# Performance work log

Measured on AMD Instinct MI355X. Metric: run time of the kernel, lower is better.

## Reference

```python
import math
import jax, jax.numpy as jnp
import numpy as np

B, T, C, H = 2, 1024, 1024, 16
D = C // H          # head_dim = 64
ROPE_M = 32         # min(head_dim//2, 64)
FB_M = 32
ROPE_BASE = 10000.0


def setup_inputs() -> dict:
    key = jax.random.key(0)
    ks = jax.random.split(key, 8)
    x = jax.random.normal(ks[0], (B, T, C), dtype=jnp.float32)
    # default coords: per-token position, d_coord=1
    coords = jnp.broadcast_to(jnp.arange(T, dtype=jnp.float32)[None, :, None], (B, T, 1))
    # c_attn / c_proj linear params (torch Linear: y = x @ W.T + b)
    W_attn = jax.random.normal(ks[1], (3 * C, C), dtype=jnp.float32) * (1.0 / math.sqrt(C))
    b_attn = jnp.zeros((3 * C,), dtype=jnp.float32)
    W_proj = jax.random.normal(ks[2], (C, C), dtype=jnp.float32) * (1.0 / math.sqrt(C))
    b_proj = jnp.zeros((C,), dtype=jnp.float32)
    # RoPE freq bank, kind='log': exp(linspace(log(1/base), 0, m)) replicated over d_coord
    steps = jnp.exp(jnp.linspace(math.log(1.0 / ROPE_BASE), 0.0, ROPE_M)).astype(jnp.float32)
    W_rope = steps[:, None]  # [m, d_coord=1]
    # Fourier-bias bank, kind='gaussian', sigma=1.0
    W_fb = jax.random.normal(ks[3], (FB_M, 1), dtype=jnp.float32)
    # betas are zero-init nn.Parameters; use small random values so bias path is exercised
    beta_cos = jax.random.normal(ks[4], (FB_M,), dtype=jnp.float32) * 0.1
    beta_sin = jax.random.normal(ks[5], (FB_M,), dtype=jnp.float32) * 0.1
    return {"x": x, "coords": coords, "W_attn": W_attn, "b_attn": b_attn,
            "W_proj": W_proj, "b_proj": b_proj, "W_rope": W_rope, "W_fb": W_fb,
            "beta_cos": beta_cos, "beta_sin": beta_sin}


def _rope_rotate(z, c, s):
    # z: [B,H,T,D]; c,s: [B,1,T,ROPE_M]; rotates first 2*ROPE_M channels pairwise
    zr = z[..., :2 * ROPE_M].reshape(*z.shape[:-1], ROPE_M, 2)
    y0 = zr[..., 0] * c - zr[..., 1] * s
    y1 = zr[..., 0] * s + zr[..., 1] * c
    y = jnp.stack((y0, y1), axis=-1).reshape(*z.shape[:-1], 2 * ROPE_M)
    return jnp.concatenate([y, z[..., 2 * ROPE_M:]], axis=-1)


def reference(x, coords, W_attn, b_attn, W_proj, b_proj, W_rope, W_fb, beta_cos, beta_sin):
    qkv = x @ W_attn.T + b_attn                      # [B,T,3C]
    q, k, v = jnp.split(qkv, 3, axis=-1)
    to_heads = lambda z: z.reshape(B, T, H, D).transpose(0, 2, 1, 3)  # [B,H,T,D]
    q, k, v = to_heads(q), to_heads(k), to_heads(v)
    # Iron RoPE: theta = coords @ W_rope.T -> [B,T,ROPE_M]
    theta = coords @ W_rope.T
    c = jnp.cos(theta)[:, None]                      # [B,1,T,ROPE_M]
    s = jnp.sin(theta)[:, None]
    q = _rope_rotate(q, c, s)
    k = _rope_rotate(k, c, s)
    att = jnp.einsum('bhqd,bhkd->bhqk', q, k) * (1.0 / math.sqrt(D))
    # relative Fourier bias (shared across heads)
    delta = coords[:, :, None, :] - coords[:, None, :, :]   # [B,Tq,Tk,1]
    S = jnp.einsum('bqkd,md->bqkm', delta, W_fb)            # [B,Tq,Tk,FB_M]
    bias = (jnp.cos(S) * beta_cos + jnp.sin(S) * beta_sin).sum(-1)  # [B,Tq,Tk]
    att = att + (1.0 / math.sqrt(FB_M)) * bias[:, None]     # [B,H,Tq,Tk]
    # non-causal: mask buffer is all ones -> no masking; dropout p=0 -> identity
    att = jax.nn.softmax(att, axis=-1)
    y = jnp.einsum('bhqk,bhkd->bhqd', att, v)
    y = y.transpose(0, 2, 1, 3).reshape(B, T, C)
    y = y @ W_proj.T + b_proj
    return x + y
```

## Files before the change

### kernel.cpp

```cpp
#include <hip/hip_runtime.h>
#include <math.h>

#define Bc 2
#define Tc 1024
#define Cc 1024
#define Hc 16
#define Dc 64
#define DE 128

typedef unsigned short u16;
typedef __attribute__((ext_vector_type(8))) short bf16x8;
typedef __attribute__((ext_vector_type(4))) float f32x4;
typedef __attribute__((ext_vector_type(16))) float f32x16;

#define QSCALE 0.1803368801111243f
#define FIXED_M 24.0f

static __device__ inline u16 f2b(float f) {
    unsigned u = __float_as_uint(f);
    u = (u + 0x7fffu + ((u >> 16) & 1u)) >> 16;
    return (u16)u;
}
static __device__ inline float b2f(u16 h) {
    return __uint_as_float((unsigned)h << 16);
}

typedef __attribute__((address_space(1))) const unsigned int g_u32;
typedef __attribute__((address_space(3))) unsigned int l_u32;
static __device__ __forceinline__ void gll16(const void* g, void* l) {
    __builtin_amdgcn_global_load_lds((g_u32*)g, (l_u32*)l, 16, 0, 0);
}

__global__ __launch_bounds__(256) void cast_all(
    const float* __restrict__ x, const float* __restrict__ wa, const float* __restrict__ wp,
    u16* __restrict__ xb, u16* __restrict__ wab, u16* __restrict__ wpb)
{
    const int NX = Bc * Tc * Cc;
    const int NA = 3 * Cc * Cc;
    int i = (blockIdx.x * 256 + threadIdx.x) * 4;
    const float* src; u16* dst; int off;
    if (i < NX)            { src = x;  dst = xb;  off = i; }
    else if (i < NX + NA)  { src = wa; dst = wab; off = i - NX; }
    else                   { src = wp; dst = wpb; off = i - NX - NA; }
    float4 v = *(const float4*)(src + off);
    ushort4 o;
    o.x = f2b(v.x); o.y = f2b(v.y); o.z = f2b(v.z); o.w = f2b(v.w);
    *(ushort4*)(dst + off) = o;
}

template<int TM, int TN, int WR, int WC, bool OUT_BF16>
__global__ __launch_bounds__(256) void gemm_abt(
    const u16* __restrict__ A, const u16* __restrict__ Bm,
    const float* __restrict__ bias, const float* __restrict__ resid,
    float* __restrict__ outf, u16* __restrict__ outb, int M, int N, int K)
{
    constexpr int WTM = TM / WR;
    constexpr int WTN = TN / WC;
    constexpr int FI = WTM / 16;
    constexpr int FJ = WTN / 16;
    constexpr int ITA = TM / 32;
    constexpr int ITB = TN / 32;
    __shared__ u16 ldsA[2][TM * 64];
    __shared__ u16 ldsB[2][TN * 64];
    const int tid  = threadIdx.x;
    const int wave = tid >> 6;
    const int lane = tid & 63;
    const int l15  = lane & 15;
    const int quad = lane >> 4;
    const int wm = wave / WC;
    const int wn = wave % WC;
    const int tm = blockIdx.y * TM;
    const int tn = blockIdx.x * TN;

    f32x4 acc[FI][FJ] = {};

    auto stage = [&](int buf, int k0) {
#pragma unroll
        for (int it = 0; it < ITA; ++it) {
            int p = it * 256 + tid;
            int row = p >> 3;
            int c = ((p & 7) ^ (row & 7)) * 8;
            gll16(A + (size_t)(tm + row) * K + k0 + c,
                  &ldsA[buf][(it * 256 + (wave << 6)) * 8]);
        }
#pragma unroll
        for (int it = 0; it < ITB; ++it) {
            int p = it * 256 + tid;
            int row = p >> 3;
            int c = ((p & 7) ^ (row & 7)) * 8;
            gll16(Bm + (size_t)(tn + row) * K + k0 + c,
                  &ldsB[buf][(it * 256 + (wave << 6)) * 8]);
        }
    };

    const int NK = K >> 6;
    stage(0, 0);
    for (int ki = 0; ki < NK; ++ki) {
        const int buf = ki & 1;
        __syncthreads();
        if (ki + 1 < NK) stage(buf ^ 1, (ki + 1) << 6);
#pragma unroll
        for (int kk = 0; kk < 2; ++kk) {
            bf16x8 af[FI], bf[FJ];
#pragma unroll
            for (int i = 0; i < FI; ++i) {
                int row = wm * WTM + i * 16 + l15;
                int slot = (kk * 4 + quad) ^ (row & 7);
                af[i] = *(const bf16x8*)&ldsA[buf][row * 64 + slot * 8];
            }
#pragma unroll
            for (int j = 0; j < FJ; ++j) {
                int row = wn * WTN + j * 16 + l15;
                int slot = (kk * 4 + quad) ^ (row & 7);
                bf[j] = *(const bf16x8*)&ldsB[buf][row * 64 + slot * 8];
            }
#pragma unroll
            for (int i = 0; i < FI; ++i)
#pragma unroll
                for (int j = 0; j < FJ; ++j)
                    acc[i][j] = __builtin_amdgcn_mfma_f32_16x16x32_bf16(af[i], bf[j], acc[i][j], 0, 0, 0);
        }
    }

#pragma unroll
    for (int i = 0; i < FI; ++i) {
        int row = tm + wm * WTM + i * 16 + quad * 4;
#pragma unroll
        for (int j = 0; j < FJ; ++j) {
            int col = tn + wn * WTN + j * 16 + l15;
            float bb = bias[col];
#pragma unroll
            for (int r = 0; r < 4; ++r) {
                float v = acc[i][j][r] + bb;
                if (resid) v += resid[(size_t)(row + r) * N + col];
                if (OUT_BF16) outb[(size_t)(row + r) * N + col] = f2b(v);
                else          outf[(size_t)(row + r) * N + col] = v;
            }
        }
    }
}

__global__ __launch_bounds__(256) void prep_kernel(
    const u16* __restrict__ qkv, const float* __restrict__ coords,
    const float* __restrict__ W_rope, const float* __restrict__ W_fb,
    const float* __restrict__ bcos, const float* __restrict__ bsin,
    u16* __restrict__ qe, u16* __restrict__ ke, u16* __restrict__ vt)
{
    const int bt = blockIdx.x;
    const int b = bt >> 10;
    const int t = bt & (Tc - 1);
    const float coord = coords[bt];
    const int tid = threadIdx.x;
    const u16* row = qkv + (size_t)bt * 3072;
    const int e  = tid * 4;
    const int h  = e >> 6;
    const int d0 = e & 63;
    const int m0 = d0 >> 1;

    float th0 = coord * W_rope[m0];
    float th1 = coord * W_rope[m0 + 1];
    float s0 = sinf(th0), c0 = cosf(th0);
    float s1 = sinf(th1), c1 = cosf(th1);

    float q0 = b2f(row[e]), q1 = b2f(row[e + 1]), q2 = b2f(row[e + 2]), q3 = b2f(row[e + 3]);
    float k0 = b2f(row[1024 + e]), k1 = b2f(row[1025 + e]), k2 = b2f(row[1026 + e]), k3 = b2f(row[1027 + e]);
    float v0 = b2f(row[2048 + e]), v1 = b2f(row[2049 + e]), v2 = b2f(row[2050 + e]), v3 = b2f(row[2051 + e]);

    size_t qb = ((size_t)(b * Hc + h) * Tc + t) * DE + d0;
    qe[qb + 0] = f2b((q0 * c0 - q1 * s0) * QSCALE);
    qe[qb + 1] = f2b((q0 * s0 + q1 * c0) * QSCALE);
    qe[qb + 2] = f2b((q2 * c1 - q3 * s1) * QSCALE);
    qe[qb + 3] = f2b((q2 * s1 + q3 * c1) * QSCALE);
    ke[qb + 0] = f2b(k0 * c0 - k1 * s0);
    ke[qb + 1] = f2b(k0 * s0 + k1 * c0);
    ke[qb + 2] = f2b(k2 * c1 - k3 * s1);
    ke[qb + 3] = f2b(k2 * s1 + k3 * c1);

    size_t vb = ((size_t)(b * Hc + h) * Dc + d0) * Tc + t;
    vt[vb]          = f2b(v0);
    vt[vb + Tc]     = f2b(v1);
    vt[vb + 2 * Tc] = f2b(v2);
    vt[vb + 3 * Tc] = f2b(v3);

    {
        const int hh = tid >> 4;
        const int s  = tid & 15;
        const int m  = 2 * s;
        float thf0 = coord * W_fb[m],     thf1 = coord * W_fb[m + 1];
        float sn0 = sinf(thf0), cn0 = cosf(thf0);
        float sn1 = sinf(thf1), cn1 = cosf(thf1);
        float bc0 = bcos[m], bs0 = bsin[m], bc1 = bcos[m + 1], bs1 = bsin[m + 1];
        const float SC = 1.41421356237f * QSCALE;
        unsigned u1 = (unsigned)f2b((bc0 * cn0 + bs0 * sn0) * SC) |
                      ((unsigned)f2b((bc1 * cn1 + bs1 * sn1) * SC) << 16);
        unsigned u2 = (unsigned)f2b((bc0 * sn0 - bs0 * cn0) * SC) |
                      ((unsigned)f2b((bc1 * sn1 - bs1 * cn1) * SC) << 16);
        unsigned cp = (unsigned)f2b(cn0) | ((unsigned)f2b(cn1) << 16);
        unsigned sp = (unsigned)f2b(sn0) | ((unsigned)f2b(sn1) << 16);
        size_t base = ((size_t)(b * Hc + hh) * Tc + t) * DE + 64;
        *(unsigned*)&qe[base + m]      = u1;
        *(unsigned*)&qe[base + 32 + m] = u2;
        *(unsigned*)&ke[base + m]      = cp;
        *(unsigned*)&ke[base + 32 + m] = sp;
    }
}

__global__ __launch_bounds__(256) void attn_kernel(
    const u16* __restrict__ qe, const u16* __restrict__ ke,
    const u16* __restrict__ vt, u16* __restrict__ yb)
{
    __shared__ u16 ldsK[2][64 * 128];
    __shared__ u16 ldsV[2][64 * 64];
    __shared__ u16 plds[4][32][40];
    __shared__ float lM[2][32];
    const int tid  = threadIdx.x;
    const int wave = tid >> 6;
    const int lane = tid & 63;
    const int l31  = lane & 31;
    const int half = lane >> 5;
    const int qw = wave & 1;
    const int kw = wave >> 1;
    const int h  = blockIdx.x & 15;
    const int b  = blockIdx.x >> 4;
    const int qt = blockIdx.y * 64;

    const u16* Q  = qe + ((size_t)(b * Hc + h) * Tc) * DE;
    const u16* Kp = ke + ((size_t)(b * Hc + h) * Tc) * DE;
    const u16* Vp = vt + ((size_t)(b * Hc + h) * Dc) * Tc;

    bf16x8 qf[8];
    {
        const u16* qrow = Q + (size_t)(qt + qw * 32 + l31) * DE + half * 8;
#pragma unroll
        for (int c = 0; c < 8; ++c) qf[c] = *(const bf16x8*)(qrow + c * 16);
    }

    auto stageKV = [&](int buf, int kt) {
#pragma unroll
        for (int it = 0; it < 4; ++it) {
            int p = it * 256 + tid;
            int row = p >> 4;
            int c = (p & 15) ^ (row & 15);
            gll16(Kp + (size_t)(kt + row) * DE + c * 8,
                  &ldsK[buf][(it * 256 + (wave << 6)) * 8]);
        }
#pragma unroll
        for (int it = 0; it < 2; ++it) {
            int p = it * 256 + tid;
            int row = p >> 3;
            int c = (p & 7) ^ (row & 7);
            gll16(Vp + (size_t)row * Tc + kt + c * 8,
                  &ldsV[buf][(it * 256 + (wave << 6)) * 8]);
        }
    };

    f32x16 o[2] = {};
    float lrow[16] = {};

    stageKV(0, 0);
    for (int ki = 0; ki < Tc / 64; ++ki) {
        const int buf = ki & 1;
        __syncthreads();
        if (ki + 1 < Tc / 64) stageKV(buf ^ 1, (ki + 1) * 64);

        f32x16 sf = {};
#pragma unroll
        for (int c = 0; c < 8; ++c) {
            int row = kw * 32 + l31;
            int slot = (c * 2 + half) ^ (row & 15);
            bf16x8 kf = *(const bf16x8*)&ldsK[buf][row * 128 + slot * 8];
            sf = __builtin_amdgcn_mfma_f32_32x32x16_bf16(qf[c], kf, sf, 0, 0, 0);
        }
#pragma unroll
        for (int r = 0; r < 16; ++r) {
            float p = __builtin_amdgcn_exp2f(sf[r] - FIXED_M);
            u16 tp = (u16)(__float_as_uint(p) >> 16);
            int row = (r & 3) + 8 * (r >> 2) + 4 * half;
            plds[wave][row][l31] = tp;
            lrow[r] += b2f(tp);
        }
#pragma unroll
        for (int kc = 0; kc < 2; ++kc) {
            bf16x8 pa = *(const bf16x8*)&plds[wave][l31][kc * 16 + half * 8];
#pragma unroll
            for (int dt = 0; dt < 2; ++dt) {
                int vrow = dt * 32 + l31;
                int chunk = (kw * 32 + kc * 16 + half * 8) >> 3;
                int slot = chunk ^ (vrow & 7);
                bf16x8 vf = *(const bf16x8*)&ldsV[buf][vrow * 64 + slot * 8];
                o[dt] = __builtin_amdgcn_mfma_f32_32x32x16_bf16(pa, vf, o[dt], 0, 0, 0);
            }
        }
    }

    __syncthreads();

#pragma unroll
    for (int r = 0; r < 16; ++r) {
        float v = lrow[r];
#pragma unroll
        for (int off = 1; off < 32; off <<= 1) v += __shfl_xor(v, off);
        lrow[r] = v;
    }

    float* oM = (float*)&ldsK[0][0];
    if (kw == 1) {
#pragma unroll
        for (int r = 0; r < 16; ++r) {
            int row = (r & 3) + 8 * (r >> 2) + 4 * half;
#pragma unroll
            for (int dt = 0; dt < 2; ++dt)
                oM[(qw * 32 + row) * 64 + dt * 32 + l31] = o[dt][r];
            if (l31 == 0) lM[qw][row] = lrow[r];
        }
    }
    __syncthreads();
    if (kw == 0) {
#pragma unroll
        for (int r = 0; r < 16; ++r) {
            int row = (r & 3) + 8 * (r >> 2) + 4 * half;
            float rl = 1.0f / (lrow[r] + lM[qw][row]);
            int t = qt + qw * 32 + row;
#pragma unroll
            for (int dt = 0; dt < 2; ++dt) {
                float val = (o[dt][r] + oM[(qw * 32 + row) * 64 + dt * 32 + l31]) * rl;
                yb[((size_t)b * Tc + t) * Cc + h * Dc + dt * 32 + l31] = f2b(val);
            }
        }
    }
}

extern "C" void kernel_launch(void* const* d_in, const int* in_sizes, int n_in,
                              void* d_out, int out_size, void* d_ws, size_t ws_size,
                              hipStream_t stream) {
    const float* x      = (const float*)d_in[0];
    const float* coords = (const float*)d_in[1];
    const float* W_attn = (const float*)d_in[2];
    const float* b_attn = (const float*)d_in[3];
    const float* W_proj = (const float*)d_in[4];
    const float* b_proj = (const float*)d_in[5];
    const float* W_rope = (const float*)d_in[6];
    const float* W_fb   = (const float*)d_in[7];
    const float* bcos   = (const float*)d_in[8];
    const float* bsin   = (const float*)d_in[9];
    float* out = (float*)d_out;

    char* w = (char*)d_ws;
    const size_t MB = 1024 * 1024;
    u16* xb     = (u16*)(w + 0);
    u16* wab    = (u16*)(w + 4 * MB);
    u16* wpb    = (u16*)(w + 10 * MB);
    u16* qkvb16 = (u16*)(w + 12 * MB);
    u16* qext   = (u16*)(w + 24 * MB);
    u16* kext   = (u16*)(w + 32 * MB);
    u16* vtw    = (u16*)(w + 40 * MB);
    u16* yb     = (u16*)(w + 44 * MB);

    const int NALL = (Bc * Tc * Cc + 3 * Cc * Cc + Cc * Cc) / 4;
    cast_all<<<NALL / 256, 256, 0, stream>>>(x, W_attn, W_proj, xb, wab, wpb);

    dim3 g1(3 * Cc / 128, Bc * Tc / 64);
    gemm_abt<64, 128, 2, 2, true><<<g1, 256, 0, stream>>>(
        xb, wab, b_attn, nullptr, nullptr, qkvb16, Bc * Tc, 3 * Cc, Cc);

    prep_kernel<<<Bc * Tc, 256, 0, stream>>>(qkvb16, coords, W_rope, W_fb, bcos, bsin, qext, kext, vtw);

    dim3 g2(Hc * Bc, Tc / 64);
    attn_kernel<<<g2, 256, 0, stream>>>(qext, kext, vtw, yb);

    dim3 g3(Cc / 64, Bc * Tc / 64);
    gemm_abt<64, 64, 2, 2, false><<<g3, 256, 0, stream>>>(
        yb, wpb, b_proj, x, out, nullptr, Bc * Tc, Cc, Cc);
}
```

Baseline: 169.6 us.

## Fuse all pipeline stages into one cooperative persistent kernel with grid syncs

Merges the cast, QKV GEMM, RoPE/bias prep, attention and output projection into a single cooperative kernel of 512 blocks, with grid-wide barriers between stages. Each stage is factored into a device tile function that shares one static shared-memory buffer. The aim is to remove four kernel-launch gaps and tail effects. In exchange, every stage is limited to 512 blocks, the QKV GEMM runs 768 tiles over 512 blocks in two uneven rounds, and each grid sync adds a global barrier. The old multi-kernel path remains as a fallback if the cooperative launch fails.

```diff
diff --git a/kernel.cpp b/kernel.cpp
--- a/kernel.cpp
+++ b/kernel.cpp
@@ -1,5 +1,8 @@
 #include <hip/hip_runtime.h>
+#include <hip/hip_cooperative_groups.h>
 #include <math.h>
+
+namespace cg = cooperative_groups;
 
 #define Bc 2
 #define Tc 1024
@@ -31,46 +34,30 @@
     __builtin_amdgcn_global_load_lds((g_u32*)g, (l_u32*)l, 16, 0, 0);
 }
 
-__global__ __launch_bounds__(256) void cast_all(
-    const float* __restrict__ x, const float* __restrict__ wa, const float* __restrict__ wp,
-    u16* __restrict__ xb, u16* __restrict__ wab, u16* __restrict__ wpb)
-{
-    const int NX = Bc * Tc * Cc;
-    const int NA = 3 * Cc * Cc;
-    int i = (blockIdx.x * 256 + threadIdx.x) * 4;
-    const float* src; u16* dst; int off;
-    if (i < NX)            { src = x;  dst = xb;  off = i; }
-    else if (i < NX + NA)  { src = wa; dst = wab; off = i - NX; }
-    else                   { src = wp; dst = wpb; off = i - NX - NA; }
-    float4 v = *(const float4*)(src + off);
-    ushort4 o;
-    o.x = f2b(v.x); o.y = f2b(v.y); o.z = f2b(v.z); o.w = f2b(v.w);
-    *(ushort4*)(dst + off) = o;
-}
-
-template<int TM, int TN, int WR, int WC, bool OUT_BF16>
-__global__ __launch_bounds__(256) void gemm_abt(
-    const u16* __restrict__ A, const u16* __restrict__ Bm,
-    const float* __restrict__ bias, const float* __restrict__ resid,
-    float* __restrict__ outf, u16* __restrict__ outb, int M, int N, int K)
-{
+
+template<int TM, int TN, bool OUT_BF16>
+__device__ __forceinline__ void gemm_tile(
+    u16* smem, int tid, int bx, int by,
+    const u16* A, const u16* Bm, const float* bias, const float* resid,
+    float* outf, u16* outb, int N, int K)
+{
+    constexpr int WR = 2, WC = 2;
     constexpr int WTM = TM / WR;
     constexpr int WTN = TN / WC;
     constexpr int FI = WTM / 16;
     constexpr int FJ = WTN / 16;
     constexpr int ITA = TM / 32;
     constexpr int ITB = TN / 32;
-    __shared__ u16 ldsA[2][TM * 64];
-    __shared__ u16 ldsB[2][TN * 64];
-    const int tid  = threadIdx.x;
+    u16* ldsA = smem;
+    u16* ldsB = smem + 2 * TM * 64;
     const int wave = tid >> 6;
     const int lane = tid & 63;
     const int l15  = lane & 15;
     const int quad = lane >> 4;
     const int wm = wave / WC;
     const int wn = wave % WC;
-    const int tm = blockIdx.y * TM;
-    const int tn = blockIdx.x * TN;
+    const int tm = by * TM;
+    const int tn = bx * TN;
 
     f32x4 acc[FI][FJ] = {};
 
@@ -81,7 +68,7 @@
             int row = p >> 3;
             int c = ((p & 7) ^ (row & 7)) * 8;
             gll16(A + (size_t)(tm + row) * K + k0 + c,
-                  &ldsA[buf][(it * 256 + (wave << 6)) * 8]);
+                  &ldsA[buf * TM * 64 + (it * 256 + (wave << 6)) * 8]);
         }
 #pragma unroll
         for (int it = 0; it < ITB; ++it) {
@@ -89,7 +76,7 @@
             int row = p >> 3;
             int c = ((p & 7) ^ (row & 7)) * 8;
             gll16(Bm + (size_t)(tn + row) * K + k0 + c,
-                  &ldsB[buf][(it * 256 + (wave << 6)) * 8]);
+                  &ldsB[buf * TN * 64 + (it * 256 + (wave << 6)) * 8]);
         }
     };
 
@@ -106,13 +93,13 @@
             for (int i = 0; i < FI; ++i) {
                 int row = wm * WTM + i * 16 + l15;
                 int slot = (kk * 4 + quad) ^ (row & 7);
-                af[i] = *(const bf16x8*)&ldsA[buf][row * 64 + slot * 8];
+                af[i] = *(const bf16x8*)&ldsA[buf * TM * 64 + row * 64 + slot * 8];
             }
 #pragma unroll
             for (int j = 0; j < FJ; ++j) {
                 int row = wn * WTN + j * 16 + l15;
                 int slot = (kk * 4 + quad) ^ (row & 7);
-                bf[j] = *(const bf16x8*)&ldsB[buf][row * 64 + slot * 8];
+                bf[j] = *(const bf16x8*)&ldsB[buf * TN * 64 + row * 64 + slot * 8];
             }
 #pragma unroll
             for (int i = 0; i < FI; ++i)
@@ -140,17 +127,16 @@
     }
 }
 
-__global__ __launch_bounds__(256) void prep_kernel(
+__device__ __forceinline__ void prep_tile(
+    int bt, int tid,
     const u16* __restrict__ qkv, const float* __restrict__ coords,
     const float* __restrict__ W_rope, const float* __restrict__ W_fb,
     const float* __restrict__ bcos, const float* __restrict__ bsin,
     u16* __restrict__ qe, u16* __restrict__ ke, u16* __restrict__ vt)
 {
-    const int bt = blockIdx.x;
     const int b = bt >> 10;
     const int t = bt & (Tc - 1);
     const float coord = coords[bt];
-    const int tid = threadIdx.x;
     const u16* row = qkv + (size_t)bt * 3072;
     const int e  = tid * 4;
     const int h  = e >> 6;
@@ -205,24 +191,23 @@
     }
 }
 
-__global__ __launch_bounds__(256) void attn_kernel(
+__device__ __forceinline__ void attn_tile(
+    char* smemc, int tid, int bid_head, int qt,
     const u16* __restrict__ qe, const u16* __restrict__ ke,
     const u16* __restrict__ vt, u16* __restrict__ yb)
 {
-    __shared__ u16 ldsK[2][64 * 128];
-    __shared__ u16 ldsV[2][64 * 64];
-    __shared__ u16 plds[4][32][40];
-    __shared__ float lM[2][32];
-    const int tid  = threadIdx.x;
+    u16*   ldsK = (u16*)smemc;
+    u16*   ldsV = (u16*)(smemc + 32768);
+    u16*   plds = (u16*)(smemc + 49152);
+    float* lM   = (float*)(smemc + 59392);
     const int wave = tid >> 6;
     const int lane = tid & 63;
     const int l31  = lane & 31;
     const int half = lane >> 5;
     const int qw = wave & 1;
     const int kw = wave >> 1;
-    const int h  = blockIdx.x & 15;
-    const int b  = blockIdx.x >> 4;
-    const int qt = blockIdx.y * 64;
+    const int h  = bid_head & 15;
+    const int b  = bid_head >> 4;
 
     const u16* Q  = qe + ((size_t)(b * Hc + h) * Tc) * DE;
     const u16* Kp = ke + ((size_t)(b * Hc + h) * Tc) * DE;
@@ -242,7 +227,7 @@
             int row = p >> 4;
             int c = (p & 15) ^ (row & 15);
             gll16(Kp + (size_t)(kt + row) * DE + c * 8,
-                  &ldsK[buf][(it * 256 + (wave << 6)) * 8]);
+                  &ldsK[buf * 8192 + (it * 256 + (wave << 6)) * 8]);
         }
 #pragma unroll
         for (int it = 0; it < 2; ++it) {
@@ -250,7 +235,7 @@
             int row = p >> 3;
             int c = (p & 7) ^ (row & 7);
             gll16(Vp + (size_t)row * Tc + kt + c * 8,
-                  &ldsV[buf][(it * 256 + (wave << 6)) * 8]);
+                  &ldsV[buf * 4096 + (it * 256 + (wave << 6)) * 8]);
         }
     };
 
@@ -268,7 +253,7 @@
         for (int c = 0; c < 8; ++c) {
             int row = kw * 32 + l31;
             int slot = (c * 2 + half) ^ (row & 15);
-            bf16x8 kf = *(const bf16x8*)&ldsK[buf][row * 128 + slot * 8];
+            bf16x8 kf = *(const bf16x8*)&ldsK[buf * 8192 + row * 128 + slot * 8];
             sf = __builtin_amdgcn_mfma_f32_32x32x16_bf16(qf[c], kf, sf, 0, 0, 0);
         }
 #pragma unroll
@@ -276,18 +261,18 @@
             float p = __builtin_amdgcn_exp2f(sf[r] - FIXED_M);
             u16 tp = (u16)(__float_as_uint(p) >> 16);
             int row = (r & 3) + 8 * (r >> 2) + 4 * half;
-            plds[wave][row][l31] = tp;
+            plds[wave * 1280 + row * 40 + l31] = tp;
             lrow[r] += b2f(tp);
         }
 #pragma unroll
         for (int kc = 0; kc < 2; ++kc) {
-            bf16x8 pa = *(const bf16x8*)&plds[wave][l31][kc * 16 + half * 8];
+            bf16x8 pa = *(const bf16x8*)&plds[wave * 1280 + l31 * 40 + kc * 16 + half * 8];
 #pragma unroll
             for (int dt = 0; dt < 2; ++dt) {
                 int vrow = dt * 32 + l31;
                 int chunk = (kw * 32 + kc * 16 + half * 8) >> 3;
                 int slot = chunk ^ (vrow & 7);
-                bf16x8 vf = *(const bf16x8*)&ldsV[buf][vrow * 64 + slot * 8];
+                bf16x8 vf = *(const bf16x8*)&ldsV[buf * 4096 + vrow * 64 + slot * 8];
                 o[dt] = __builtin_amdgcn_mfma_f32_32x32x16_bf16(pa, vf, o[dt], 0, 0, 0);
             }
         }
@@ -303,7 +288,7 @@
         lrow[r] = v;
     }
 
-    float* oM = (float*)&ldsK[0][0];
+    float* oM = (float*)smemc;
     if (kw == 1) {
 #pragma unroll
         for (int r = 0; r < 16; ++r) {
@@ -311,7 +296,7 @@
 #pragma unroll
             for (int dt = 0; dt < 2; ++dt)
                 oM[(qw * 32 + row) * 64 + dt * 32 + l31] = o[dt][r];
-            if (l31 == 0) lM[qw][row] = lrow[r];
+            if (l31 == 0) lM[qw * 32 + row] = lrow[r];
         }
     }
     __syncthreads();
@@ -319,7 +304,7 @@
 #pragma unroll
         for (int r = 0; r < 16; ++r) {
             int row = (r & 3) + 8 * (r >> 2) + 4 * half;
-            float rl = 1.0f / (lrow[r] + lM[qw][row]);
+            float rl = 1.0f / (lrow[r] + lM[qw * 32 + row]);
             int t = qt + qw * 32 + row;
 #pragma unroll
             for (int dt = 0; dt < 2; ++dt) {
@@ -328,6 +313,101 @@
             }
         }
     }
+}
+
+__global__ __launch_bounds__(256, 2) void mega(
+    const float* __restrict__ x, const float* __restrict__ coords,
+    const float* __restrict__ W_attn, const float* __restrict__ b_attn,
+    const float* __restrict__ W_proj, const float* __restrict__ b_proj,
+    const float* __restrict__ W_rope, const float* __restrict__ W_fb,
+    const float* __restrict__ bcos, const float* __restrict__ bsin,
+    float* __restrict__ out,
+    u16* xb, u16* wab, u16* wpb, u16* qkvb16,
+    u16* qe, u16* ke, u16* vt, u16* yb)
+{
+    __shared__ __align__(16) char smemc[59648];
+    u16* smem = (u16*)smemc;
+    cg::grid_group gg = cg::this_grid();
+    const int bid = blockIdx.x;
+    const int tid = threadIdx.x;
+
+    {
+        const int NX = Bc * Tc * Cc;
+        const int NA = 3 * Cc * Cc;
+#pragma unroll
+        for (int j = 0; j < 12; ++j) {
+            int i = ((j * 512 + bid) * 256 + tid) * 4;
+            const float* src; u16* dst; int off;
+            if (i < NX)           { src = x;      dst = xb;  off = i; }
+            else if (i < NX + NA) { src = W_attn; dst = wab; off = i - NX; }
+            else                  { src = W_proj; dst = wpb; off = i - NX - NA; }
+            float4 v = *(const float4*)(src + off);
+            ushort4 o;
+            o.x = f2b(v.x); o.y = f2b(v.y); o.z = f2b(v.z); o.w = f2b(v.w);
+            *(ushort4*)(dst + off) = o;
+        }
+    }
+    gg.sync();
+
+    for (int t = bid; t < 768; t += 512)
+        gemm_tile<64, 128, true>(smem, tid, t % 24, t / 24,
+                                 xb, wab, b_attn, nullptr, nullptr, qkvb16, 3 * Cc, Cc);
+    gg.sync();
+
+    for (int bt = bid; bt < Bc * Tc; bt += 512)
+        prep_tile(bt, tid, qkvb16, coords, W_rope, W_fb, bcos, bsin, qe, ke, vt);
+    gg.sync();
+
+    attn_tile(smemc, tid, bid & 31, (bid >> 5) * 64, qe, ke, vt, yb);
+    gg.sync();
+
+    gemm_tile<64, 64, false>(smem, tid, bid & 15, bid >> 4,
+                             yb, wpb, b_proj, x, out, nullptr, Cc, Cc);
+}
+
+__global__ __launch_bounds__(256) void cast_all(
+    const float* __restrict__ x, const float* __restrict__ wa, const float* __restrict__ wp,
+    u16* __restrict__ xb, u16* __restrict__ wab, u16* __restrict__ wpb)
+{
+    const int NX = Bc * Tc * Cc;
+    const int NA = 3 * Cc * Cc;
+    int i = (blockIdx.x * 256 + threadIdx.x) * 4;
+    const float* src; u16* dst; int off;
+    if (i < NX)            { src = x;  dst = xb;  off = i; }
+    else if (i < NX + NA)  { src = wa; dst = wab; off = i - NX; }
+    else                   { src = wp; dst = wpb; off = i - NX - NA; }
+    float4 v = *(const float4*)(src + off);
+    ushort4 o;
+    o.x = f2b(v.x); o.y = f2b(v.y); o.z = f2b(v.z); o.w = f2b(v.w);
+    *(ushort4*)(dst + off) = o;
+}
+
+template<int TM, int TN, bool OUT_BF16>
+__global__ __launch_bounds__(256) void gemm_abt(
+    const u16* __restrict__ A, const u16* __restrict__ Bm,
+    const float* __restrict__ bias, const float* __restrict__ resid,
+    float* __restrict__ outf, u16* __restrict__ outb, int N, int K)
+{
+    __shared__ u16 smem[2 * TM * 64 + 2 * TN * 64];
+    gemm_tile<TM, TN, OUT_BF16>(smem, threadIdx.x, blockIdx.x, blockIdx.y,
+                                A, Bm, bias, resid, outf, outb, N, K);
+}
+
+__global__ __launch_bounds__(256) void prep_kernel(
+    const u16* __restrict__ qkv, const float* __restrict__ coords,
+    const float* __restrict__ W_rope, const float* __restrict__ W_fb,
+    const float* __restrict__ bcos, const float* __restrict__ bsin,
+    u16* __restrict__ qe, u16* __restrict__ ke, u16* __restrict__ vt)
+{
+    prep_tile(blockIdx.x, threadIdx.x, qkv, coords, W_rope, W_fb, bcos, bsin, qe, ke, vt);
+}
+
+__global__ __launch_bounds__(256) void attn_kernel(
+    const u16* __restrict__ qe, const u16* __restrict__ ke,
+    const u16* __restrict__ vt, u16* __restrict__ yb)
+{
+    __shared__ __align__(16) char smemc[59648];
+    attn_tile(smemc, threadIdx.x, blockIdx.x & 31, (blockIdx.x >> 5) * 64, qe, ke, vt, yb);
 }
 
 extern "C" void kernel_launch(void* const* d_in, const int* in_sizes, int n_in,
@@ -356,19 +436,26 @@
     u16* vtw    = (u16*)(w + 40 * MB);
     u16* yb     = (u16*)(w + 44 * MB);
 
-    const int NALL = (Bc * Tc * Cc + 3 * Cc * Cc + Cc * Cc) / 4;
-    cast_all<<<NALL / 256, 256, 0, stream>>>(x, W_attn, W_proj, xb, wab, wpb);
-
-    dim3 g1(3 * Cc / 128, Bc * Tc / 64);
-    gemm_abt<64, 128, 2, 2, true><<<g1, 256, 0, stream>>>(
-        xb, wab, b_attn, nullptr, nullptr, qkvb16, Bc * Tc, 3 * Cc, Cc);
-
-    prep_kernel<<<Bc * Tc, 256, 0, stream>>>(qkvb16, coords, W_rope, W_fb, bcos, bsin, qext, kext, vtw);
-
-    dim3 g2(Hc * Bc, Tc / 64);
-    attn_kernel<<<g2, 256, 0, stream>>>(qext, kext, vtw, yb);
-
-    dim3 g3(Cc / 64, Bc * Tc / 64);
-    gemm_abt<64, 64, 2, 2, false><<<g3, 256, 0, stream>>>(
-        yb, wpb, b_proj, x, out, nullptr, Bc * Tc, Cc, Cc);
-}
+    void* args[] = { &x, &coords, &W_attn, &b_attn, &W_proj, &b_proj,
+                     &W_rope, &W_fb, &bcos, &bsin, &out,
+                     &xb, &wab, &wpb, &qkvb16, &qext, &kext, &vtw, &yb };
+    hipError_t e = hipLaunchCooperativeKernel((const void*)mega, dim3(512), dim3(256),
+                                              args, 0, stream);
+    if (e != hipSuccess) {
+        const int NALL = (Bc * Tc * Cc + 3 * Cc * Cc + Cc * Cc) / 4;
+        cast_all<<<NALL / 256, 256, 0, stream>>>(x, W_attn, W_proj, xb, wab, wpb);
+
+        dim3 g1(3 * Cc / 128, Bc * Tc / 64);
+        gemm_abt<64, 128, true><<<g1, 256, 0, stream>>>(
+            xb, wab, b_attn, nullptr, nullptr, qkvb16, 3 * Cc, Cc);
+
+        prep_kernel<<<Bc * Tc, 256, 0, stream>>>(qkvb16, coords, W_rope, W_fb,
+                                                 bcos, bsin, qext, kext, vtw);
+
+        attn_kernel<<<dim3(512), 256, 0, stream>>>(qext, kext, vtw, yb);
+
+        dim3 g3(Cc / 64, Bc * Tc / 64);
+        gemm_abt<64, 64, false><<<g3, 256, 0, stream>>>(
+            yb, wpb, b_proj, x, out, nullptr, Cc, Cc);
+    }
+}
```

Measured after the change: 429.2 us. 153% more time.
